# Performance work log

Hardware: AMD Instinct MI355X
Metric: run time of the kernel (lower is better)

Reference implementation:

```python
import jax, jax.numpy as jnp
import numpy as np

D_MODEL = 1024
NUM_HEADS = 16
THETA = 10000.0


def setup_inputs() -> dict:
    key = jax.random.key(0)
    ks = jax.random.split(key, 5)
    B, S, D = 4, 2048, D_MODEL
    std = float(np.sqrt(2.0 / (D + D)))
    x = jax.random.normal(ks[0], (B, S, D), dtype=jnp.float32)
    wq = jax.random.normal(ks[1], (D, D), dtype=jnp.float32) * std
    wk = jax.random.normal(ks[2], (D, D), dtype=jnp.float32) * std
    wv = jax.random.normal(ks[3], (D, D), dtype=jnp.float32) * std
    wo = jax.random.normal(ks[4], (D, D), dtype=jnp.float32) * std
    token_positions = jnp.broadcast_to(jnp.arange(S, dtype=jnp.int32), (B, S))
    return {"x": x, "token_positions": token_positions,
            "wq": wq, "wk": wk, "wv": wv, "wo": wo}


def _rope(t, token_positions, d_k):
    # t: [B, H, S, d_k]; token_positions: [B, S]
    freqs = 1.0 / (THETA ** (jnp.arange(0, d_k, 2, dtype=jnp.float32) / d_k))  # [d_k/2]
    angles = token_positions.astype(jnp.float32)[..., None] * freqs            # [B, S, d_k/2]
    angles = jnp.repeat(angles, 2, axis=-1)                                    # [B, S, d_k]
    cos = jnp.cos(angles)[:, None, :, :]  # broadcast over heads
    sin = jnp.sin(angles)[:, None, :, :]
    t1, t2 = t[..., 0::2], t[..., 1::2]
    t_rot = jnp.stack([-t2, t1], axis=-1).reshape(t.shape)  # interleave (-x2, x1)
    return t * cos + t_rot * sin


def reference(x, token_positions, wq, wk, wv, wo):
    B, S, D = x.shape
    H = NUM_HEADS
    d_k = D // H
    def proj(w):
        return (x @ w.T).reshape(B, S, H, d_k).transpose(0, 2, 1, 3)  # [B,H,S,dk]
    q = _rope(proj(wq), token_positions, d_k)
    k = _rope(proj(wk), token_positions, d_k)
    v = proj(wv)
    scale = 1.0 / jnp.sqrt(jnp.float32(d_k))
    scores = jnp.einsum('bhqd,bhkd->bhqk', q, k) * scale  # [B,H,S,S]
    causal = jnp.tril(jnp.ones((S, S), dtype=bool))
    scores = jnp.where(causal, scores, -jnp.inf)
    attn = jax.nn.softmax(scores, axis=-1)
    out = jnp.einsum('bhqk,bhkd->bhqd', attn, v)          # [B,H,S,dk]
    out = out.transpose(0, 2, 1, 3).reshape(B, S, D)
    return out @ wo.T
```

## Files before the change

kernel.cpp:

```cpp
#include <hip/hip_runtime.h>
#include <hip/hip_bf16.h>
#include <cstdint>
#include <cstddef>

#define B_ 4
#define S_ 2048
#define D_ 1024
#define H_ 16
#define DK_ 64
#define NTOK (B_*S_)

typedef __bf16 bf16;
typedef __bf16 bf16x8 __attribute__((ext_vector_type(8)));
typedef short s16x4 __attribute__((ext_vector_type(4)));
typedef float f32x4 __attribute__((ext_vector_type(4)));

#define AS1 __attribute__((address_space(1)))
#define AS3 __attribute__((address_space(3)))

static __device__ __forceinline__ short f2bf_s(float f) {
    return __builtin_bit_cast(short, (__bf16)f);
}

static __device__ __forceinline__ f32x4 mfma16(s16x4 a, s16x4 b, f32x4 c) {
#if __has_builtin(__builtin_amdgcn_mfma_f32_16x16x16bf16_1k)
    return __builtin_amdgcn_mfma_f32_16x16x16bf16_1k(a, b, c, 0, 0, 0);
#else
    asm volatile("v_mfma_f32_16x16x16_bf16 %0, %1, %2, %0\n\ts_nop 7\n\ts_nop 7"
                 : "+v"(c) : "v"(a), "v"(b));
    return c;
#endif
}

__global__ void cvt_all(const float* __restrict__ x, const float* __restrict__ wq,
                        const float* __restrict__ wk, const float* __restrict__ wv,
                        const float* __restrict__ wo, bf16* __restrict__ dst) {
    const int NX8 = NTOK * D_ / 8;
    const int W8 = D_ * D_ / 8;
    int i = blockIdx.x * blockDim.x + threadIdx.x;
    if (i >= NX8 + 4 * W8) return;
    const float* src; int j;
    if (i < NX8) { src = x; j = i; }
    else {
        int k = i - NX8;
        int w = k >> 17;
        j = k & (W8 - 1);
        src = w == 0 ? wq : (w == 1 ? wk : (w == 2 ? wv : wo));
    }
    const float4* s4 = reinterpret_cast<const float4*>(src) + (size_t)j * 2;
    float4 a = s4[0], b = s4[1];
    bf16x8 o;
    o[0] = (bf16)a.x; o[1] = (bf16)a.y; o[2] = (bf16)a.z; o[3] = (bf16)a.w;
    o[4] = (bf16)b.x; o[5] = (bf16)b.y; o[6] = (bf16)b.z; o[7] = (bf16)b.w;
    reinterpret_cast<bf16x8*>(dst)[i] = o;
}

__global__ void rope_table(const int* __restrict__ pos, float2* __restrict__ tab) {
    int i = blockIdx.x * blockDim.x + threadIdx.x;
    if (i >= NTOK * 32) return;
    int n = i >> 5, p = i & 31;
    float pf = (float)pos[n];
    float freq = powf(10000.0f, -(float)p * (1.0f / 32.0f));
    float ang = pf * freq;
    float s, c;
    sincosf(ang, &s, &c);
    tab[i] = make_float2(c, s);
}

template<int MODE>
__global__ __launch_bounds__(256, 2)
void gemm128(const bf16* __restrict__ A, const bf16* __restrict__ Bw,
             void* __restrict__ OutP, const float2* __restrict__ tab) {
    const float SCL2E = 0.125f * 1.44269504088896340736f;
    constexpr int NKT = 16;
    __shared__ alignas(16) bf16 lds[2][(128 + 128) * 64];
    const int tid = threadIdx.x;
    const int lane = tid & 63;
    const int wid = tid >> 6;
    const int wm = wid >> 1;
    const int wn = wid & 1;
    const int lr = lane & 15, lg = lane >> 4;
    const int m0 = blockIdx.x * 128;
    const int n0g = blockIdx.y * 128;

    f32x4 acc[4][4] = {};

    auto stage = [&](int kt, int bufi) {
        bf16* dst = &lds[bufi][0];
#pragma unroll
        for (int j = 0; j < 4; ++j) {
            int flat = j * 256 + tid;
            int r = flat >> 3, c = flat & 7;
            const bf16* src = A + (size_t)(m0 + r) * 1024 + kt * 64 + ((c ^ (r & 7)) << 3);
            __builtin_amdgcn_global_load_lds((const AS1 uint32_t*)src,
                                             (AS3 uint32_t*)(dst + (size_t)flat * 8), 16, 0, 0);
        }
#pragma unroll
        for (int j = 0; j < 4; ++j) {
            int flat = j * 256 + tid;
            int r = flat >> 3, c = flat & 7;
            const bf16* src = Bw + (size_t)(n0g + r) * 1024 + kt * 64 + ((c ^ (r & 7)) << 3);
            __builtin_amdgcn_global_load_lds((const AS1 uint32_t*)src,
                                             (AS3 uint32_t*)(dst + 128 * 64 + (size_t)flat * 8), 16, 0, 0);
        }
    };

    stage(0, 0);

    for (int kt = 0; kt < NKT; ++kt) {
        const bf16* bufA = &lds[kt & 1][0];
        const bf16* bufB = bufA + 128 * 64;

        asm volatile("" ::: "memory");
        __builtin_amdgcn_s_barrier();
        asm volatile("" ::: "memory");
        if (kt + 1 < NKT) {
            stage(kt + 1, (kt + 1) & 1);
            asm volatile("s_waitcnt vmcnt(8)" ::: "memory");
        } else {
            asm volatile("s_waitcnt vmcnt(0)" ::: "memory");
        }
        __builtin_amdgcn_s_barrier();
        asm volatile("" ::: "memory");

        const int sx = lr & 7;
        bf16x8 af[4][2], bfr[4][2];
#pragma unroll
        for (int mf = 0; mf < 4; ++mf)
#pragma unroll
            for (int kh = 0; kh < 2; ++kh)
                af[mf][kh] = *reinterpret_cast<const bf16x8*>(
                    &bufA[(wm * 64 + mf * 16 + lr) * 64 + (((kh * 4 + lg) ^ sx) << 3)]);
#pragma unroll
        for (int nf = 0; nf < 4; ++nf)
#pragma unroll
            for (int kh = 0; kh < 2; ++kh)
                bfr[nf][kh] = *reinterpret_cast<const bf16x8*>(
                    &bufB[(wn * 64 + nf * 16 + lr) * 64 + (((kh * 4 + lg) ^ sx) << 3)]);
        __builtin_amdgcn_s_setprio(1);
#pragma unroll
        for (int mf = 0; mf < 4; ++mf)
#pragma unroll
            for (int nf = 0; nf < 4; ++nf)
#pragma unroll
                for (int kh = 0; kh < 2; ++kh)
                    acc[mf][nf] = __builtin_amdgcn_mfma_f32_16x16x32_bf16(af[mf][kh], bfr[nf][kh], acc[mf][nf], 0, 0, 0);
        __builtin_amdgcn_s_setprio(0);
    }

#pragma unroll
    for (int mf = 0; mf < 4; ++mf) {
#pragma unroll
        for (int nf = 0; nf < 4; ++nf) {
#pragma unroll
            for (int r = 0; r < 4; ++r) {
                int row = m0 + wm * 64 + mf * 16 + lg * 4 + r;
                int colg = n0g + wn * 64 + nf * 16 + lr;
                float v = acc[mf][nf][r];
                if (MODE == 2) {
                    ((float*)OutP)[(size_t)row * 1024 + colg] = v;
                } else {
                    int which = colg >> 10;
                    int col = colg & 1023;
                    bf16* O = (bf16*)OutP + (size_t)which * NTOK * D_;
                    if (which < 2) {
                        float partner = __shfl_xor(v, 1, 64);
                        float2 cs = tab[(size_t)row * 32 + ((col >> 1) & 31)];
                        float o = (col & 1) ? fmaf(v, cs.x, partner * cs.y)
                                            : fmaf(v, cs.x, -partner * cs.y);
                        if (which == 0) o *= SCL2E;
                        O[(size_t)row * D_ + col] = (bf16)o;
                    } else {
                        O[(size_t)row * D_ + col] = (bf16)v;
                    }
                }
            }
        }
    }
}

__global__ __launch_bounds__(256, 2)
void flash_attn5(const bf16* __restrict__ Q, const bf16* __restrict__ Kr,
                 const bf16* __restrict__ V, bf16* __restrict__ O) {
    __shared__ bf16 Ks[2][64 * 64];
    __shared__ bf16 Vt[2][64 * 64];
    const int tid = threadIdx.x, lane = tid & 63, w = tid >> 6;
    const int lr = lane & 15, lg = lane >> 4;
    const int qtA = blockIdx.x;
    const int qtB = 15 - qtA;
    const int q0[2] = { qtA * 128, qtB * 128 };
    const int ntS[2] = { 2 * qtA + 2, 2 * qtB + 2 };
    const int NT = ntS[1];
    const int bh = blockIdx.y;
    const int b = bh >> 4, h = bh & 15;
    const size_t base = ((size_t)b * S_) * D_ + (size_t)h * DK_;

    bf16x8 aq[2][2][2];
#pragma unroll
    for (int si = 0; si < 2; ++si)
#pragma unroll
        for (int qs = 0; qs < 2; ++qs) {
            int qrow = q0[si] + w * 32 + qs * 16 + lr;
            const bf16* qp = Q + base + (size_t)qrow * D_ + lg * 8;
            aq[si][qs][0] = *reinterpret_cast<const bf16x8*>(qp);
            aq[si][qs][1] = *reinterpret_cast<const bf16x8*>(qp + 32);
        }

    f32x4 acc[2][2][4] = {};
    float m_run[2][2] = {{-1e30f, -1e30f}, {-1e30f, -1e30f}};
    float l_run[2][2] = {{0.f, 0.f}, {0.f, 0.f}};

    const int sjj = tid >> 3;
    const int se0 = (tid & 7) * 8;
    const int vx = tid & 7;
    bf16x8 kreg[2], vreg[2];
#pragma unroll
    for (int i = 0; i < 2; ++i) {
        int row = sjj + i * 32;
        kreg[i] = *reinterpret_cast<const bf16x8*>(&Kr[base + (size_t)row * D_ + se0]);
        vreg[i] = *reinterpret_cast<const bf16x8*>(&V [base + (size_t)row * D_ + se0]);
    }

    for (int t = 0; t < NT; ++t) {
        const int j0 = t * 64;
        bf16* KsB = Ks[t & 1];
        bf16* VtB = Vt[t & 1];
#pragma unroll
        for (int i = 0; i < 2; ++i) {
            int jj = sjj + i * 32;
            *reinterpret_cast<bf16x8*>(&KsB[jj * 64 + (se0 ^ ((jj & 7) << 3))]) = kreg[i];
#pragma unroll
            for (int q = 0; q < 8; ++q) {
                int dd = se0 + q;
                int vswz = ((q ^ vx) & 7) << 3;
                VtB[dd * 64 + (jj ^ vswz)] = vreg[i][q];
            }
        }
        if (t + 1 < NT) {
#pragma unroll
            for (int i = 0; i < 2; ++i) {
                int row = (t + 1) * 64 + sjj + i * 32;
                kreg[i] = *reinterpret_cast<const bf16x8*>(&Kr[base + (size_t)row * D_ + se0]);
                vreg[i] = *reinterpret_cast<const bf16x8*>(&V [base + (size_t)row * D_ + se0]);
            }
        }
        __syncthreads();

#pragma unroll
        for (int si = 0; si < 2; ++si) {
            if (t >= ntS[si]) continue;
            const int qmaxw = q0[si] + w * 32 + 31;
            if (j0 > qmaxw) continue;

            f32x4 sc[2][4];
            __builtin_amdgcn_s_setprio(1);
#pragma unroll
            for (int nt = 0; nt < 4; ++nt) {
                int krow = nt * 16 + lr;
                int swz = (krow & 7) << 3;
                bf16x8 a0 = *reinterpret_cast<const bf16x8*>(&KsB[krow * 64 + ((lg * 8) ^ swz)]);
                bf16x8 a1 = *reinterpret_cast<const bf16x8*>(&KsB[krow * 64 + ((32 + lg * 8) ^ swz)]);
#pragma unroll
                for (int qs = 0; qs < 2; ++qs) {
                    f32x4 tv = {};
                    tv = __builtin_amdgcn_mfma_f32_16x16x32_bf16(a0, aq[si][qs][0], tv, 0, 0, 0);
                    tv = __builtin_amdgcn_mfma_f32_16x16x32_bf16(a1, aq[si][qs][1], tv, 0, 0, 0);
                    sc[qs][nt] = tv;
                }
            }
            __builtin_amdgcn_s_setprio(0);

            s16x4 ap[2][4];
#pragma unroll
            for (int qs = 0; qs < 2; ++qs) {
                const int qrow = q0[si] + w * 32 + qs * 16 + lr;
                if (j0 + 63 > q0[si] + w * 32 + qs * 16) {
#pragma unroll
                    for (int nt = 0; nt < 4; ++nt)
#pragma unroll
                        for (int r = 0; r < 4; ++r) {
                            int kv = j0 + nt * 16 + lg * 4 + r;
                            if (kv > qrow) sc[qs][nt][r] = -1e30f;
                        }
                }
                float tmax = sc[qs][0][0];
#pragma unroll
                for (int nt = 0; nt < 4; ++nt)
#pragma unroll
                    for (int r = 0; r < 4; ++r) tmax = fmaxf(tmax, sc[qs][nt][r]);
                tmax = fmaxf(tmax, __shfl_xor(tmax, 16, 64));
                tmax = fmaxf(tmax, __shfl_xor(tmax, 32, 64));
                float mold = m_run[si][qs];
                if (!__all(tmax - mold <= 8.0f)) {
                    float mnew = fmaxf(mold, tmax);
                    float corr = exp2f(mold - mnew);
                    m_run[si][qs] = mnew;
                    l_run[si][qs] *= corr;
#pragma unroll
                    for (int r = 0; r < 4; ++r) {
                        float cr = __shfl(corr, (lane & 48) | (lg * 4 + r), 64);
#pragma unroll
                        for (int dt = 0; dt < 4; ++dt) acc[si][qs][dt][r] *= cr;
                    }
                }
                float mnow = m_run[si][qs];
                float rs = 0.f;
#pragma unroll
                for (int nt = 0; nt < 4; ++nt)
#pragma unroll
                    for (int r = 0; r < 4; ++r) {
                        float p = exp2f(sc[qs][nt][r] - mnow);
                        rs += p;
                        ap[qs][nt][r] = f2bf_s(p);
                    }
                rs += __shfl_xor(rs, 16, 64);
                rs += __shfl_xor(rs, 32, 64);
                l_run[si][qs] += rs;
            }

            __builtin_amdgcn_s_setprio(1);
#pragma unroll
            for (int dt = 0; dt < 4; ++dt) {
                int vrow = dt * 16 + lr;
                int vswz = (((vrow & 7) ^ (vrow >> 3)) & 7) << 3;
                s16x4 bv[4];
#pragma unroll
                for (int nt = 0; nt < 4; ++nt)
                    bv[nt] = *reinterpret_cast<const s16x4*>(&VtB[vrow * 64 + ((nt * 16 + lg * 4) ^ vswz)]);
#pragma unroll
                for (int qs = 0; qs < 2; ++qs)
#pragma unroll
                    for (int nt = 0; nt < 4; ++nt)
                        acc[si][qs][dt] = mfma16(ap[qs][nt], bv[nt], acc[si][qs][dt]);
            }
            __builtin_amdgcn_s_setprio(0);
        }
    }

#pragma unroll
    for (int si = 0; si < 2; ++si)
#pragma unroll
        for (int qs = 0; qs < 2; ++qs) {
            float inv = __builtin_amdgcn_rcpf(l_run[si][qs]);
#pragma unroll
            for (int r = 0; r < 4; ++r) {
                float invr = __shfl(inv, (lane & 48) | (lg * 4 + r), 64);
                int row = q0[si] + w * 32 + qs * 16 + lg * 4 + r;
#pragma unroll
                for (int dt = 0; dt < 4; ++dt)
                    O[base + (size_t)row * D_ + dt * 16 + lr] = (bf16)(acc[si][qs][dt][r] * invr);
            }
        }
}

extern "C" void kernel_launch(void* const* d_in, const int* in_sizes, int n_in,
                              void* d_out, int out_size, void* d_ws, size_t ws_size,
                              hipStream_t stream) {
    const float* x  = (const float*)d_in[0];
    const int*   tp = (const int*)d_in[1];
    const float* wq = (const float*)d_in[2];
    const float* wk = (const float*)d_in[3];
    const float* wv = (const float*)d_in[4];
    const float* wo = (const float*)d_in[5];

    bf16* ws = (bf16*)d_ws;
    bf16* Xbf = ws;
    bf16* Wqb = Xbf + (size_t)NTOK * D_;
    bf16* Wkb = Wqb + (size_t)D_ * D_;
    bf16* Wvb = Wkb + (size_t)D_ * D_;
    bf16* Wob = Wvb + (size_t)D_ * D_;
    bf16* Qr  = Wob + (size_t)D_ * D_;
    bf16* Kb  = Qr + (size_t)NTOK * D_;
    bf16* Vb  = Kb + (size_t)NTOK * D_;
    bf16* AO  = Vb + (size_t)NTOK * D_;
    float2* tab = (float2*)(AO + (size_t)NTOK * D_);
    (void)ws_size; (void)in_sizes; (void)n_in; (void)out_size;
    (void)Wkb; (void)Wvb;

    {
        int ntot8 = (NTOK * D_ + 4 * D_ * D_) / 8;
        cvt_all<<<(ntot8 + 255) / 256, 256, 0, stream>>>(x, wq, wk, wv, wo, Xbf);
    }
    rope_table<<<(NTOK * 32 + 255) / 256, 256, 0, stream>>>(tp, tab);

    gemm128<1><<<dim3(NTOK / 128, 24), 256, 0, stream>>>(Xbf, Wqb, Qr, tab);

    flash_attn5<<<dim3(8, B_ * H_), 256, 0, stream>>>(Qr, Kb, Vb, AO);

    gemm128<2><<<dim3(NTOK / 128, D_ / 128), 256, 0, stream>>>(AO, Wob, d_out, nullptr);
}
```

Baseline: 206.3 us.

## Halve flash-attention query tile to 64 rows and double grid blocks

Each attention block now pairs two 64-row query tiles (s and 31-s) instead of two 128-row tiles, and each wave owns 16 query rows instead of 32. The grid doubles from 8 to 16 blocks per batch-head, giving 1024 blocks instead of 512, for better CU occupancy and load balance on the causal triangle. The cost is that every K/V tile is loaded and staged into shared memory by twice as many blocks, so each K/V load feeds fewer MFMAs.

Result: slower. 212.8 us (+3.1%).

```diff
diff --git a/kernel.cpp b/kernel.cpp
--- a/kernel.cpp
+++ b/kernel.cpp
@@ -180,35 +180,33 @@
 }
 
 __global__ __launch_bounds__(256, 2)
-void flash_attn5(const bf16* __restrict__ Q, const bf16* __restrict__ Kr,
+void flash_attn8(const bf16* __restrict__ Q, const bf16* __restrict__ Kr,
                  const bf16* __restrict__ V, bf16* __restrict__ O) {
     __shared__ bf16 Ks[2][64 * 64];
     __shared__ bf16 Vt[2][64 * 64];
     const int tid = threadIdx.x, lane = tid & 63, w = tid >> 6;
     const int lr = lane & 15, lg = lane >> 4;
-    const int qtA = blockIdx.x;
-    const int qtB = 15 - qtA;
-    const int q0[2] = { qtA * 128, qtB * 128 };
-    const int ntS[2] = { 2 * qtA + 2, 2 * qtB + 2 };
+    const int bx = blockIdx.x;
+    const int sA = bx, sB = 31 - bx;
+    const int q0[2] = { sA * 64, sB * 64 };
+    const int ntS[2] = { sA + 1, sB + 1 };
     const int NT = ntS[1];
     const int bh = blockIdx.y;
     const int b = bh >> 4, h = bh & 15;
     const size_t base = ((size_t)b * S_) * D_ + (size_t)h * DK_;
 
-    bf16x8 aq[2][2][2];
-#pragma unroll
-    for (int si = 0; si < 2; ++si)
-#pragma unroll
-        for (int qs = 0; qs < 2; ++qs) {
-            int qrow = q0[si] + w * 32 + qs * 16 + lr;
-            const bf16* qp = Q + base + (size_t)qrow * D_ + lg * 8;
-            aq[si][qs][0] = *reinterpret_cast<const bf16x8*>(qp);
-            aq[si][qs][1] = *reinterpret_cast<const bf16x8*>(qp + 32);
-        }
-
-    f32x4 acc[2][2][4] = {};
-    float m_run[2][2] = {{-1e30f, -1e30f}, {-1e30f, -1e30f}};
-    float l_run[2][2] = {{0.f, 0.f}, {0.f, 0.f}};
+    bf16x8 aq[2][2];
+#pragma unroll
+    for (int si = 0; si < 2; ++si) {
+        int qrow = q0[si] + w * 16 + lr;
+        const bf16* qp = Q + base + (size_t)qrow * D_ + lg * 8;
+        aq[si][0] = *reinterpret_cast<const bf16x8*>(qp);
+        aq[si][1] = *reinterpret_cast<const bf16x8*>(qp + 32);
+    }
+
+    f32x4 acc[2][4] = {};
+    float m_run[2] = {-1e30f, -1e30f};
+    float l_run[2] = {0.f, 0.f};
 
     const int sjj = tid >> 3;
     const int se0 = (tid & 7) * 8;
@@ -249,10 +247,10 @@
 #pragma unroll
         for (int si = 0; si < 2; ++si) {
             if (t >= ntS[si]) continue;
-            const int qmaxw = q0[si] + w * 32 + 31;
-            if (j0 > qmaxw) continue;
-
-            f32x4 sc[2][4];
+            const int qrow0 = q0[si] + w * 16;
+            if (j0 > qrow0 + 15) continue;
+
+            f32x4 sc[4];
             __builtin_amdgcn_s_setprio(1);
 #pragma unroll
             for (int nt = 0; nt < 4; ++nt) {
@@ -260,63 +258,57 @@
                 int swz = (krow & 7) << 3;
                 bf16x8 a0 = *reinterpret_cast<const bf16x8*>(&KsB[krow * 64 + ((lg * 8) ^ swz)]);
                 bf16x8 a1 = *reinterpret_cast<const bf16x8*>(&KsB[krow * 64 + ((32 + lg * 8) ^ swz)]);
-#pragma unroll
-                for (int qs = 0; qs < 2; ++qs) {
-                    f32x4 tv = {};
-                    tv = __builtin_amdgcn_mfma_f32_16x16x32_bf16(a0, aq[si][qs][0], tv, 0, 0, 0);
-                    tv = __builtin_amdgcn_mfma_f32_16x16x32_bf16(a1, aq[si][qs][1], tv, 0, 0, 0);
-                    sc[qs][nt] = tv;
+                f32x4 tv = {};
+                tv = __builtin_amdgcn_mfma_f32_16x16x32_bf16(a0, aq[si][0], tv, 0, 0, 0);
+                tv = __builtin_amdgcn_mfma_f32_16x16x32_bf16(a1, aq[si][1], tv, 0, 0, 0);
+                sc[nt] = tv;
+            }
+            __builtin_amdgcn_s_setprio(0);
+
+            const int qrow = qrow0 + lr;
+            if (j0 + 63 > qrow0) {
+#pragma unroll
+                for (int nt = 0; nt < 4; ++nt)
+#pragma unroll
+                    for (int r = 0; r < 4; ++r) {
+                        int kv = j0 + nt * 16 + lg * 4 + r;
+                        if (kv > qrow) sc[nt][r] = -1e30f;
+                    }
+            }
+            float tmax = sc[0][0];
+#pragma unroll
+            for (int nt = 0; nt < 4; ++nt)
+#pragma unroll
+                for (int r = 0; r < 4; ++r) tmax = fmaxf(tmax, sc[nt][r]);
+            tmax = fmaxf(tmax, __shfl_xor(tmax, 16, 64));
+            tmax = fmaxf(tmax, __shfl_xor(tmax, 32, 64));
+            float mold = m_run[si];
+            if (!__all(tmax - mold <= 8.0f)) {
+                float mnew = fmaxf(mold, tmax);
+                float corr = exp2f(mold - mnew);
+                m_run[si] = mnew;
+                l_run[si] *= corr;
+#pragma unroll
+                for (int r = 0; r < 4; ++r) {
+                    float cr = __shfl(corr, (lane & 48) | (lg * 4 + r), 64);
+#pragma unroll
+                    for (int dt = 0; dt < 4; ++dt) acc[si][dt][r] *= cr;
                 }
             }
-            __builtin_amdgcn_s_setprio(0);
-
-            s16x4 ap[2][4];
-#pragma unroll
-            for (int qs = 0; qs < 2; ++qs) {
-                const int qrow = q0[si] + w * 32 + qs * 16 + lr;
-                if (j0 + 63 > q0[si] + w * 32 + qs * 16) {
-#pragma unroll
-                    for (int nt = 0; nt < 4; ++nt)
-#pragma unroll
-                        for (int r = 0; r < 4; ++r) {
-                            int kv = j0 + nt * 16 + lg * 4 + r;
-                            if (kv > qrow) sc[qs][nt][r] = -1e30f;
-                        }
+            float mnow = m_run[si];
+            s16x4 ap[4];
+            float rs = 0.f;
+#pragma unroll
+            for (int nt = 0; nt < 4; ++nt)
+#pragma unroll
+                for (int r = 0; r < 4; ++r) {
+                    float p = exp2f(sc[nt][r] - mnow);
+                    rs += p;
+                    ap[nt][r] = f2bf_s(p);
                 }
-                float tmax = sc[qs][0][0];
-#pragma unroll
-                for (int nt = 0; nt < 4; ++nt)
-#pragma unroll
-                    for (int r = 0; r < 4; ++r) tmax = fmaxf(tmax, sc[qs][nt][r]);
-                tmax = fmaxf(tmax, __shfl_xor(tmax, 16, 64));
-                tmax = fmaxf(tmax, __shfl_xor(tmax, 32, 64));
-                float mold = m_run[si][qs];
-                if (!__all(tmax - mold <= 8.0f)) {
-                    float mnew = fmaxf(mold, tmax);
-                    float corr = exp2f(mold - mnew);
-                    m_run[si][qs] = mnew;
-                    l_run[si][qs] *= corr;
-#pragma unroll
-                    for (int r = 0; r < 4; ++r) {
-                        float cr = __shfl(corr, (lane & 48) | (lg * 4 + r), 64);
-#pragma unroll
-                        for (int dt = 0; dt < 4; ++dt) acc[si][qs][dt][r] *= cr;
-                    }
-                }
-                float mnow = m_run[si][qs];
-                float rs = 0.f;
-#pragma unroll
-                for (int nt = 0; nt < 4; ++nt)
-#pragma unroll
-                    for (int r = 0; r < 4; ++r) {
-                        float p = exp2f(sc[qs][nt][r] - mnow);
-                        rs += p;
-                        ap[qs][nt][r] = f2bf_s(p);
-                    }
-                rs += __shfl_xor(rs, 16, 64);
-                rs += __shfl_xor(rs, 32, 64);
-                l_run[si][qs] += rs;
-            }
+            rs += __shfl_xor(rs, 16, 64);
+            rs += __shfl_xor(rs, 32, 64);
+            l_run[si] += rs;
 
             __builtin_amdgcn_s_setprio(1);
 #pragma unroll
@@ -328,29 +320,25 @@
                 for (int nt = 0; nt < 4; ++nt)
                     bv[nt] = *reinterpret_cast<const s16x4*>(&VtB[vrow * 64 + ((nt * 16 + lg * 4) ^ vswz)]);
 #pragma unroll
-                for (int qs = 0; qs < 2; ++qs)
-#pragma unroll
-                    for (int nt = 0; nt < 4; ++nt)
-                        acc[si][qs][dt] = mfma16(ap[qs][nt], bv[nt], acc[si][qs][dt]);
+                for (int nt = 0; nt < 4; ++nt)
+                    acc[si][dt] = mfma16(ap[nt], bv[nt], acc[si][dt]);
             }
             __builtin_amdgcn_s_setprio(0);
         }
     }
 
 #pragma unroll
-    for (int si = 0; si < 2; ++si)
-#pragma unroll
-        for (int qs = 0; qs < 2; ++qs) {
-            float inv = __builtin_amdgcn_rcpf(l_run[si][qs]);
-#pragma unroll
-            for (int r = 0; r < 4; ++r) {
-                float invr = __shfl(inv, (lane & 48) | (lg * 4 + r), 64);
-                int row = q0[si] + w * 32 + qs * 16 + lg * 4 + r;
-#pragma unroll
-                for (int dt = 0; dt < 4; ++dt)
-                    O[base + (size_t)row * D_ + dt * 16 + lr] = (bf16)(acc[si][qs][dt][r] * invr);
-            }
-        }
+    for (int si = 0; si < 2; ++si) {
+        float inv = __builtin_amdgcn_rcpf(l_run[si]);
+#pragma unroll
+        for (int r = 0; r < 4; ++r) {
+            float invr = __shfl(inv, (lane & 48) | (lg * 4 + r), 64);
+            int row = q0[si] + w * 16 + lg * 4 + r;
+#pragma unroll
+            for (int dt = 0; dt < 4; ++dt)
+                O[base + (size_t)row * D_ + dt * 16 + lr] = (bf16)(acc[si][dt][r] * invr);
+        }
+    }
 }
 
 extern "C" void kernel_launch(void* const* d_in, const int* in_sizes, int n_in,
@@ -385,7 +373,7 @@
 
     gemm128<1><<<dim3(NTOK / 128, 24), 256, 0, stream>>>(Xbf, Wqb, Qr, tab);
 
-    flash_attn5<<<dim3(8, B_ * H_), 256, 0, stream>>>(Qr, Kb, Vb, AO);
+    flash_attn8<<<dim3(16, B_ * H_), 256, 0, stream>>>(Qr, Kb, Vb, AO);
 
     gemm128<2><<<dim3(NTOK / 128, D_ / 128), 256, 0, stream>>>(AO, Wob, d_out, nullptr);
 }
```

## Emit pre-swizzled K and transposed V from QKV GEMM; async-load tiles in attention

Applied to the files above, without the earlier changes.

The QKV projection epilogue now writes K with the LDS XOR swizzle already applied and writes V pre-transposed into per-(batch,head,tile) swizzled blocks. The attention kernel can then copy K/V tiles straight to LDS with global_load_lds double buffering. This removes the register round trip and the scalar transposing scatter stores into LDS. The cost is scattered 8-byte V stores in the GEMM epilogue and a layout coupling between the two kernels. The GEMM template is split into two separate kernels.

Result: slower. 214.0 us (+3.7%).

```diff
diff --git a/kernel.cpp b/kernel.cpp
--- a/kernel.cpp
+++ b/kernel.cpp
@@ -67,18 +67,17 @@
     tab[i] = make_float2(c, s);
 }
 
-template<int MODE>
 __global__ __launch_bounds__(256, 2)
-void gemm128(const bf16* __restrict__ A, const bf16* __restrict__ Bw,
-             void* __restrict__ OutP, const float2* __restrict__ tab) {
+void gemm_qkv(const bf16* __restrict__ A, const bf16* __restrict__ Bw,
+              bf16* __restrict__ Qr, bf16* __restrict__ Kz, bf16* __restrict__ VT,
+              const float2* __restrict__ tab) {
     const float SCL2E = 0.125f * 1.44269504088896340736f;
     constexpr int NKT = 16;
     __shared__ alignas(16) bf16 lds[2][(128 + 128) * 64];
     const int tid = threadIdx.x;
     const int lane = tid & 63;
     const int wid = tid >> 6;
-    const int wm = wid >> 1;
-    const int wn = wid & 1;
+    const int wm = wid >> 1, wn = wid & 1;
     const int lr = lane & 15, lg = lane >> 4;
     const int m0 = blockIdx.x * 128;
     const int n0g = blockIdx.y * 128;
@@ -152,36 +151,135 @@
     for (int mf = 0; mf < 4; ++mf) {
 #pragma unroll
         for (int nf = 0; nf < 4; ++nf) {
+            int row0 = m0 + wm * 64 + mf * 16 + lg * 4;
+            int colg = n0g + wn * 64 + nf * 16 + lr;
+            int which = colg >> 10;
+            int col = colg & 1023;
+            if (which < 2) {
+#pragma unroll
+                for (int r = 0; r < 4; ++r) {
+                    int row = row0 + r;
+                    float v = acc[mf][nf][r];
+                    float partner = __shfl_xor(v, 1, 64);
+                    float2 cs = tab[(size_t)row * 32 + ((col >> 1) & 31)];
+                    float o = (col & 1) ? fmaf(v, cs.x, partner * cs.y)
+                                        : fmaf(v, cs.x, -partner * cs.y);
+                    if (which == 0) {
+                        Qr[(size_t)row * 1024 + col] = (bf16)(o * SCL2E);
+                    } else {
+                        int h = col >> 6, e = col & 63;
+                        int e2 = e ^ ((row & 7) << 3);
+                        Kz[(size_t)row * 1024 + h * 64 + e2] = (bf16)o;
+                    }
+                }
+            } else {
+                int h = col >> 6, dd = col & 63;
+                int kvb = row0 & 63;
+                int sw = (((dd & 7) ^ ((dd >> 3) & 7)) & 7) << 3;
+                s16x4 pk;
+#pragma unroll
+                for (int r = 0; r < 4; ++r) pk[r] = f2bf_s(acc[mf][nf][r]);
+                size_t addr = ((((size_t)((row0 >> 11) * 16 + h)) * 32 + ((row0 >> 6) & 31)) * 64 + dd) * 64
+                              + (size_t)(kvb ^ sw);
+                *reinterpret_cast<s16x4*>(&VT[addr]) = pk;
+            }
+        }
+    }
+}
+
+__global__ __launch_bounds__(256, 2)
+void gemm_out(const bf16* __restrict__ A, const bf16* __restrict__ Bw,
+              float* __restrict__ Cp) {
+    constexpr int NKT = 16;
+    __shared__ alignas(16) bf16 lds[2][(128 + 128) * 64];
+    const int tid = threadIdx.x;
+    const int lane = tid & 63;
+    const int wid = tid >> 6;
+    const int wm = wid >> 1, wn = wid & 1;
+    const int lr = lane & 15, lg = lane >> 4;
+    const int m0 = blockIdx.x * 128;
+    const int n0g = blockIdx.y * 128;
+
+    f32x4 acc[4][4] = {};
+
+    auto stage = [&](int kt, int bufi) {
+        bf16* dst = &lds[bufi][0];
+#pragma unroll
+        for (int j = 0; j < 4; ++j) {
+            int flat = j * 256 + tid;
+            int r = flat >> 3, c = flat & 7;
+            const bf16* src = A + (size_t)(m0 + r) * 1024 + kt * 64 + ((c ^ (r & 7)) << 3);
+            __builtin_amdgcn_global_load_lds((const AS1 uint32_t*)src,
+                                             (AS3 uint32_t*)(dst + (size_t)flat * 8), 16, 0, 0);
+        }
+#pragma unroll
+        for (int j = 0; j < 4; ++j) {
+            int flat = j * 256 + tid;
+            int r = flat >> 3, c = flat & 7;
+            const bf16* src = Bw + (size_t)(n0g + r) * 1024 + kt * 64 + ((c ^ (r & 7)) << 3);
+            __builtin_amdgcn_global_load_lds((const AS1 uint32_t*)src,
+                                             (AS3 uint32_t*)(dst + 128 * 64 + (size_t)flat * 8), 16, 0, 0);
+        }
+    };
+
+    stage(0, 0);
+
+    for (int kt = 0; kt < NKT; ++kt) {
+        const bf16* bufA = &lds[kt & 1][0];
+        const bf16* bufB = bufA + 128 * 64;
+
+        asm volatile("" ::: "memory");
+        __builtin_amdgcn_s_barrier();
+        asm volatile("" ::: "memory");
+        if (kt + 1 < NKT) {
+            stage(kt + 1, (kt + 1) & 1);
+            asm volatile("s_waitcnt vmcnt(8)" ::: "memory");
+        } else {
+            asm volatile("s_waitcnt vmcnt(0)" ::: "memory");
+        }
+        __builtin_amdgcn_s_barrier();
+        asm volatile("" ::: "memory");
+
+        const int sx = lr & 7;
+        bf16x8 af[4][2], bfr[4][2];
+#pragma unroll
+        for (int mf = 0; mf < 4; ++mf)
+#pragma unroll
+            for (int kh = 0; kh < 2; ++kh)
+                af[mf][kh] = *reinterpret_cast<const bf16x8*>(
+                    &bufA[(wm * 64 + mf * 16 + lr) * 64 + (((kh * 4 + lg) ^ sx) << 3)]);
+#pragma unroll
+        for (int nf = 0; nf < 4; ++nf)
+#pragma unroll
+            for (int kh = 0; kh < 2; ++kh)
+                bfr[nf][kh] = *reinterpret_cast<const bf16x8*>(
+                    &bufB[(wn * 64 + nf * 16 + lr) * 64 + (((kh * 4 + lg) ^ sx) << 3)]);
+        __builtin_amdgcn_s_setprio(1);
+#pragma unroll
+        for (int mf = 0; mf < 4; ++mf)
+#pragma unroll
+            for (int nf = 0; nf < 4; ++nf)
+#pragma unroll
+                for (int kh = 0; kh < 2; ++kh)
+                    acc[mf][nf] = __builtin_amdgcn_mfma_f32_16x16x32_bf16(af[mf][kh], bfr[nf][kh], acc[mf][nf], 0, 0, 0);
+        __builtin_amdgcn_s_setprio(0);
+    }
+
+#pragma unroll
+    for (int mf = 0; mf < 4; ++mf)
+#pragma unroll
+        for (int nf = 0; nf < 4; ++nf)
 #pragma unroll
             for (int r = 0; r < 4; ++r) {
                 int row = m0 + wm * 64 + mf * 16 + lg * 4 + r;
                 int colg = n0g + wn * 64 + nf * 16 + lr;
-                float v = acc[mf][nf][r];
-                if (MODE == 2) {
-                    ((float*)OutP)[(size_t)row * 1024 + colg] = v;
-                } else {
-                    int which = colg >> 10;
-                    int col = colg & 1023;
-                    bf16* O = (bf16*)OutP + (size_t)which * NTOK * D_;
-                    if (which < 2) {
-                        float partner = __shfl_xor(v, 1, 64);
-                        float2 cs = tab[(size_t)row * 32 + ((col >> 1) & 31)];
-                        float o = (col & 1) ? fmaf(v, cs.x, partner * cs.y)
-                                            : fmaf(v, cs.x, -partner * cs.y);
-                        if (which == 0) o *= SCL2E;
-                        O[(size_t)row * D_ + col] = (bf16)o;
-                    } else {
-                        O[(size_t)row * D_ + col] = (bf16)v;
-                    }
-                }
-            }
-        }
-    }
+                Cp[(size_t)row * 1024 + colg] = acc[mf][nf][r];
+            }
 }
 
 __global__ __launch_bounds__(256, 2)
-void flash_attn5(const bf16* __restrict__ Q, const bf16* __restrict__ Kr,
-                 const bf16* __restrict__ V, bf16* __restrict__ O) {
+void flash_attn9(const bf16* __restrict__ Q, const bf16* __restrict__ Kz,
+                 const bf16* __restrict__ VT, bf16* __restrict__ O) {
     __shared__ bf16 Ks[2][64 * 64];
     __shared__ bf16 Vt[2][64 * 64];
     const int tid = threadIdx.x, lane = tid & 63, w = tid >> 6;
@@ -194,6 +292,7 @@
     const int bh = blockIdx.y;
     const int b = bh >> 4, h = bh & 15;
     const size_t base = ((size_t)b * S_) * D_ + (size_t)h * DK_;
+    const size_t vtbase = (size_t)bh * 32 * 4096;
 
     bf16x8 aq[2][2][2];
 #pragma unroll
@@ -212,39 +311,40 @@
 
     const int sjj = tid >> 3;
     const int se0 = (tid & 7) * 8;
-    const int vx = tid & 7;
-    bf16x8 kreg[2], vreg[2];
-#pragma unroll
-    for (int i = 0; i < 2; ++i) {
-        int row = sjj + i * 32;
-        kreg[i] = *reinterpret_cast<const bf16x8*>(&Kr[base + (size_t)row * D_ + se0]);
-        vreg[i] = *reinterpret_cast<const bf16x8*>(&V [base + (size_t)row * D_ + se0]);
-    }
+
+    auto stage = [&](int t, int bufi) {
+        bf16* kd = Ks[bufi];
+        bf16* vd = Vt[bufi];
+#pragma unroll
+        for (int i = 0; i < 2; ++i) {
+            int jj = sjj + i * 32;
+            const bf16* ksrc = Kz + base + (size_t)(t * 64 + jj) * 1024 + se0;
+            __builtin_amdgcn_global_load_lds((const AS1 uint32_t*)ksrc,
+                                             (AS3 uint32_t*)(kd + jj * 64 + se0), 16, 0, 0);
+            const bf16* vsrc = VT + vtbase + (size_t)t * 4096 + jj * 64 + se0;
+            __builtin_amdgcn_global_load_lds((const AS1 uint32_t*)vsrc,
+                                             (AS3 uint32_t*)(vd + jj * 64 + se0), 16, 0, 0);
+        }
+    };
+
+    stage(0, 0);
 
     for (int t = 0; t < NT; ++t) {
         const int j0 = t * 64;
-        bf16* KsB = Ks[t & 1];
-        bf16* VtB = Vt[t & 1];
-#pragma unroll
-        for (int i = 0; i < 2; ++i) {
-            int jj = sjj + i * 32;
-            *reinterpret_cast<bf16x8*>(&KsB[jj * 64 + (se0 ^ ((jj & 7) << 3))]) = kreg[i];
-#pragma unroll
-            for (int q = 0; q < 8; ++q) {
-                int dd = se0 + q;
-                int vswz = ((q ^ vx) & 7) << 3;
-                VtB[dd * 64 + (jj ^ vswz)] = vreg[i][q];
-            }
-        }
+        const bf16* KsB = Ks[t & 1];
+        const bf16* VtB = Vt[t & 1];
+
+        asm volatile("" ::: "memory");
+        __builtin_amdgcn_s_barrier();
+        asm volatile("" ::: "memory");
         if (t + 1 < NT) {
-#pragma unroll
-            for (int i = 0; i < 2; ++i) {
-                int row = (t + 1) * 64 + sjj + i * 32;
-                kreg[i] = *reinterpret_cast<const bf16x8*>(&Kr[base + (size_t)row * D_ + se0]);
-                vreg[i] = *reinterpret_cast<const bf16x8*>(&V [base + (size_t)row * D_ + se0]);
-            }
-        }
-        __syncthreads();
+            stage(t + 1, (t + 1) & 1);
+            asm volatile("s_waitcnt vmcnt(4)" ::: "memory");
+        } else {
+            asm volatile("s_waitcnt vmcnt(0)" ::: "memory");
+        }
+        __builtin_amdgcn_s_barrier();
+        asm volatile("" ::: "memory");
 
 #pragma unroll
         for (int si = 0; si < 2; ++si) {
@@ -370,9 +470,9 @@
     bf16* Wvb = Wkb + (size_t)D_ * D_;
     bf16* Wob = Wvb + (size_t)D_ * D_;
     bf16* Qr  = Wob + (size_t)D_ * D_;
-    bf16* Kb  = Qr + (size_t)NTOK * D_;
-    bf16* Vb  = Kb + (size_t)NTOK * D_;
-    bf16* AO  = Vb + (size_t)NTOK * D_;
+    bf16* Kz  = Qr + (size_t)NTOK * D_;
+    bf16* VT  = Kz + (size_t)NTOK * D_;
+    bf16* AO  = VT + (size_t)NTOK * D_;
     float2* tab = (float2*)(AO + (size_t)NTOK * D_);
     (void)ws_size; (void)in_sizes; (void)n_in; (void)out_size;
     (void)Wkb; (void)Wvb;
@@ -383,9 +483,9 @@
     }
     rope_table<<<(NTOK * 32 + 255) / 256, 256, 0, stream>>>(tp, tab);
 
-    gemm128<1><<<dim3(NTOK / 128, 24), 256, 0, stream>>>(Xbf, Wqb, Qr, tab);
-
-    flash_attn5<<<dim3(8, B_ * H_), 256, 0, stream>>>(Qr, Kb, Vb, AO);
-
-    gemm128<2><<<dim3(NTOK / 128, D_ / 128), 256, 0, stream>>>(AO, Wob, d_out, nullptr);
-}
+    gemm_qkv<<<dim3(NTOK / 128, 24), 256, 0, stream>>>(Xbf, Wqb, Qr, Kz, VT, tab);
+
+    flash_attn9<<<dim3(8, B_ * H_), 256, 0, stream>>>(Qr, Kz, VT, AO);
+
+    gemm_out<<<dim3(NTOK / 128, D_ / 128), 256, 0, stream>>>(AO, Wob, (float*)d_out);
+}
```
